# Optimization experiments

Hardware: AMD Instinct MI355X
Metric: run time of the kernel (lower is better)

The kernel has to match this reference:

```python
import jax, jax.numpy as jnp
import numpy as np

T = 16          # timesteps
BATCH = 8       # video clips -> leading dim of x is BATCH*T = 128
C_IN = 768      # fixed by nn.Conv2d(768, redu_dim, 1)
D = 256         # redu_dim
K = 64          # num_centers
H = W = 28
EPS = 1e-12     # torch F.normalize eps


def _conv(x, w, padding):
    # x: [N,C,H,W], w: [O,I,kh,kw]
    return jax.lax.conv_general_dilated(
        x, w, window_strides=(1, 1), padding=padding,
        dimension_numbers=('NCHW', 'OIHW', 'NCHW'))


def setup_inputs() -> dict:
    key = jax.random.key(0)
    ks = jax.random.split(key, 9)
    x = jax.random.normal(ks[0], (BATCH * T, C_IN, H, W), dtype=jnp.float32)
    redu_w = jax.random.normal(ks[1], (D, C_IN, 1, 1), jnp.float32) * 0.02
    redu_b = jnp.zeros((D,), jnp.float32)
    share_w = jax.random.normal(ks[2], (K, D, 1, 1), jnp.float32) * 0.05
    share_b = jnp.zeros((K,), jnp.float32)
    U_z = jax.random.normal(ks[3], (K, K, 3, 3), jnp.float32) * 0.04
    U_r = jax.random.normal(ks[4], (K, K, 3, 3), jnp.float32) * 0.04
    U_h = jax.random.normal(ks[5], (K, K, 3, 3), jnp.float32) * 0.04
    centers = jax.random.normal(ks[6], (K, D), jnp.float32) * 0.06
    return {"x": x, "redu_w": redu_w, "redu_b": redu_b,
            "share_w": share_w, "share_b": share_b,
            "U_z": U_z, "U_r": U_r, "U_h": U_h,
            "centers": centers, "timesteps": T}


def reference(x, redu_w, redu_b, share_w, share_b, U_z, U_r, U_h, centers, timesteps):
    t = timesteps
    bt, _, h, w = x.shape
    b = bt // t
    k = share_w.shape[0]
    d = redu_w.shape[0]

    # channel reduction (1x1 conv)
    xr = _conv(x, redu_w, 'VALID') + redu_b[None, :, None, None]        # [bt,d,h,w]
    # shared assignment logits (1x1 conv)
    wxb = _conv(xr, share_w, 'VALID') + share_b[None, :, None, None]     # [bt,k,h,w]
    wxb = wxb.reshape(b, t, k, h, w).transpose(1, 0, 2, 3, 4)            # [t,b,k,h,w]

    # sequential ConvGRU over timesteps
    h0 = jnp.zeros((b, k, h, w), x.dtype)
    def step(h_tm1, w_t):
        z = jax.nn.sigmoid(w_t + _conv(h_tm1, U_z, 'SAME'))
        r = jax.nn.sigmoid(w_t + _conv(h_tm1, U_r, 'SAME'))
        hh = jnp.tanh(w_t + _conv(r * h_tm1, U_h, 'SAME'))
        h_new = (1.0 - z) * hh + z * h_tm1
        return h_new, h_new
    _, hs = jax.lax.scan(step, h0, wxb)                                  # [t,b,k,h,w]

    assign = hs.transpose(1, 0, 2, 3, 4).reshape(b * t, k, h * w)        # [bt,k,hw]
    # softmax over centers per spatial location
    assign = jax.nn.softmax(assign, axis=1)

    # VLAD aggregation
    a_sum = assign.sum(axis=-1, keepdims=True)                           # [bt,k,1]
    a = a_sum * centers[None]                                            # [bt,k,d]
    xf = xr.reshape(b * t, d, h * w)                                     # [bt,d,hw]
    vlad = jnp.einsum('bkp,bdp->bkd', assign, xf) - a                    # [bt,k,d]

    vlad = vlad.reshape(b, t, k, d).sum(axis=1)                          # [b,k,d]
    # intra-norm over feature dim, then global L2 norm
    vlad = vlad / jnp.maximum(jnp.linalg.norm(vlad, axis=2, keepdims=True), EPS)
    vlad = vlad.reshape(b, k * d)
    vlad = vlad / jnp.maximum(jnp.linalg.norm(vlad, axis=1, keepdims=True), EPS)
    return vlad
```

## Files before the change

### kernel.cpp

```cpp
#include <hip/hip_runtime.h>
#include <hip/hip_bf16.h>

#define T_ 16
#define B_ 8
#define CIN 768
#define D_ 256
#define K_ 64
#define HW 784
#define W_ 28

typedef short short8 __attribute__((ext_vector_type(8)));
typedef short short4v __attribute__((ext_vector_type(4)));
typedef float floatx4 __attribute__((ext_vector_type(4)));
typedef unsigned short ushort_t;

__device__ __forceinline__ unsigned short f2bf(float x) {
    union { float f; unsigned u; } v; v.f = x;
    unsigned u = v.u;
    unsigned r = (u + 0x7fffu + ((u >> 16) & 1u)) >> 16;
    return (unsigned short)r;
}
__device__ __forceinline__ float bf2f(unsigned short h) {
    union { unsigned u; float f; } v; v.u = ((unsigned)h) << 16; return v.f;
}

__device__ __forceinline__ float block_reduce_sum_256(float v) {
    for (int off = 32; off > 0; off >>= 1) v += __shfl_down(v, off, 64);
    __shared__ float red[4];
    __shared__ float tot;
    int lane = threadIdx.x & 63, wid = threadIdx.x >> 6;
    if (lane == 0) red[wid] = v;
    __syncthreads();
    if (threadIdx.x == 0) tot = red[0] + red[1] + red[2] + red[3];
    __syncthreads();
    return tot;
}

__global__ __launch_bounds__(256) void cvt_weights(
    const float* __restrict__ rw, const float* __restrict__ sw,
    const float* __restrict__ Uz, const float* __restrict__ Ur,
    const float* __restrict__ Uh,
    ushort_t* __restrict__ whi, ushort_t* __restrict__ wlo,
    ushort_t* __restrict__ shi, ushort_t* __restrict__ slo,
    ushort_t* __restrict__ azh, ushort_t* __restrict__ azl,
    ushort_t* __restrict__ ahh, ushort_t* __restrict__ ahl)
{
    int i = blockIdx.x * 256 + threadIdx.x;
    const int nR = D_ * CIN;
    const int nS = K_ * D_;
    const int nZR = 128 * 576;
    const int nH = 64 * 576;
    if (i < nR) {
        float x = rw[i];
        unsigned short h = f2bf(x);
        whi[i] = h; wlo[i] = f2bf(x - bf2f(h));
    } else if (i < nR + nS) {
        int j = i - nR;
        float x = sw[j];
        unsigned short h = f2bf(x);
        shi[j] = h; slo[j] = f2bf(x - bf2f(h));
    } else if (i < nR + nS + nZR) {
        int j = i - nR - nS;
        int row = j / 576, kk = j - row * 576;
        int tap = kk >> 6, c = kk & 63;
        const float* U = (row < 64) ? Uz : Ur;
        float x = U[(((size_t)(row & 63)) * 64 + c) * 9 + tap];
        unsigned short h = f2bf(x);
        azh[j] = h; azl[j] = f2bf(x - bf2f(h));
    } else if (i < nR + nS + nZR + nH) {
        int j = i - nR - nS - nZR;
        int row = j / 576, kk = j - row * 576;
        int tap = kk >> 6, c = kk & 63;
        float x = Uh[(((size_t)row) * 64 + c) * 9 + tap];
        unsigned short h = f2bf(x);
        ahh[j] = h; ahl[j] = f2bf(x - bf2f(h));
    }
}

template<int BM, int KD>
__global__ __launch_bounds__(256, 2) void mfma_conv1x1(
    const float* __restrict__ X, const ushort_t* __restrict__ Whi,
    const ushort_t* __restrict__ Wlo, const float* __restrict__ bias,
    float* __restrict__ Out)
{
    const int nt = blockIdx.x, bt = blockIdx.z;
    const int p0 = nt * 112;
    const int tid = threadIdx.x, lane = tid & 63, wv = tid >> 6;
    const float* Xb = X + (size_t)bt * KD * HW;
    float* Ob = Out + (size_t)bt * BM * HW;

    __shared__ ushort_t lB[2][112 * 40];

    constexpr int NI = (BM == 256) ? 7 : 2;
    constexpr int NKS = KD / 32;
    floatx4 acc[4][NI];
#pragma unroll
    for (int a = 0; a < 4; ++a)
#pragma unroll
        for (int b = 0; b < NI; ++b) acc[a][b] = (floatx4){0.f, 0.f, 0.f, 0.f};

    const int koff = (lane >> 4) * 8;
    const int li = lane & 15;
    const int mbase = (BM == 256) ? wv * 64 : 0;

    const int u0j = tid / 112, u0p = tid - u0j * 112;
    const bool u1v = tid < 192;
    const int u1j = (tid + 256) / 112, u1p = (tid + 256) - u1j * 112;

    float b0[16], b1[16];
    short8 ahi[4], alo[4];

    auto loadB = [&](int k0, float* bb) {
        const float* xp0 = Xb + (size_t)(k0 + u0j * 8) * HW + p0 + u0p;
#pragma unroll
        for (int c = 0; c < 8; ++c) bb[c] = xp0[c * HW];
        if (u1v) {
            const float* xp1 = Xb + (size_t)(k0 + u1j * 8) * HW + p0 + u1p;
#pragma unroll
            for (int c = 0; c < 8; ++c) bb[8 + c] = xp1[c * HW];
        }
    };
    auto writeB = [&](const float* bb) {
        short8 vh, vl;
#pragma unroll
        for (int c = 0; c < 8; ++c) {
            unsigned short h = f2bf(bb[c]);
            vh[c] = (short)h; vl[c] = (short)f2bf(bb[c] - bf2f(h));
        }
        *(short8*)&lB[0][u0p * 40 + u0j * 8] = vh;
        *(short8*)&lB[1][u0p * 40 + u0j * 8] = vl;
        if (u1v) {
#pragma unroll
            for (int c = 0; c < 8; ++c) {
                unsigned short h = f2bf(bb[8 + c]);
                vh[c] = (short)h; vl[c] = (short)f2bf(bb[8 + c] - bf2f(h));
            }
            *(short8*)&lB[0][u1p * 40 + u1j * 8] = vh;
            *(short8*)&lB[1][u1p * 40 + u1j * 8] = vl;
        }
    };
    auto loadA = [&](int k0) {
#pragma unroll
        for (int mi = 0; mi < 4; ++mi) {
            int m = mbase + mi * 16 + li;
            ahi[mi] = *(const short8*)(Whi + (size_t)m * KD + k0 + koff);
            alo[mi] = *(const short8*)(Wlo + (size_t)m * KD + k0 + koff);
        }
    };
    auto domfma = [&]() {
        if constexpr (BM == 256) {
#pragma unroll
            for (int ni = 0; ni < 7; ++ni) {
                int n = ni * 16 + li;
                short8 bhi = *(const short8*)&lB[0][n * 40 + koff];
                short8 blo = *(const short8*)&lB[1][n * 40 + koff];
#pragma unroll
                for (int mi = 0; mi < 4; ++mi) {
                    acc[mi][ni] = __builtin_amdgcn_mfma_f32_16x16x32_bf16(ahi[mi], bhi, acc[mi][ni], 0, 0, 0);
                    acc[mi][ni] = __builtin_amdgcn_mfma_f32_16x16x32_bf16(ahi[mi], blo, acc[mi][ni], 0, 0, 0);
                    acc[mi][ni] = __builtin_amdgcn_mfma_f32_16x16x32_bf16(alo[mi], bhi, acc[mi][ni], 0, 0, 0);
                }
            }
        } else {
#pragma unroll
            for (int nj = 0; nj < 2; ++nj) {
                int ni = wv * 2 + nj;
                if (ni >= 7) break;
                int n = ni * 16 + li;
                short8 bhi = *(const short8*)&lB[0][n * 40 + koff];
                short8 blo = *(const short8*)&lB[1][n * 40 + koff];
#pragma unroll
                for (int mi = 0; mi < 4; ++mi) {
                    acc[mi][nj] = __builtin_amdgcn_mfma_f32_16x16x32_bf16(ahi[mi], bhi, acc[mi][nj], 0, 0, 0);
                    acc[mi][nj] = __builtin_amdgcn_mfma_f32_16x16x32_bf16(ahi[mi], blo, acc[mi][nj], 0, 0, 0);
                    acc[mi][nj] = __builtin_amdgcn_mfma_f32_16x16x32_bf16(alo[mi], bhi, acc[mi][nj], 0, 0, 0);
                }
            }
        }
    };

    loadB(0, b0);
    for (int ks = 0; ks < NKS; ks += 2) {
        loadA(ks * 32);
        writeB(b0);
        __syncthreads();
        if (ks + 1 < NKS) loadB((ks + 1) * 32, b1);
        domfma();
        __syncthreads();
        loadA((ks + 1) * 32);
        writeB(b1);
        __syncthreads();
        if (ks + 2 < NKS) loadB((ks + 2) * 32, b0);
        domfma();
        __syncthreads();
    }

    if constexpr (BM == 256) {
#pragma unroll
        for (int mi = 0; mi < 4; ++mi) {
            int m0g = wv * 64 + mi * 16 + ((lane >> 4) << 2);
#pragma unroll
            for (int ni = 0; ni < 7; ++ni) {
                int p = p0 + ni * 16 + li;
#pragma unroll
                for (int r = 0; r < 4; ++r)
                    Ob[(size_t)(m0g + r) * HW + p] = acc[mi][ni][r] + bias[m0g + r];
            }
        }
    } else {
#pragma unroll
        for (int nj = 0; nj < 2; ++nj) {
            int ni = wv * 2 + nj;
            if (ni >= 7) break;
            int p = p0 + ni * 16 + li;
#pragma unroll
            for (int mi = 0; mi < 4; ++mi) {
                int m0g = mi * 16 + ((lane >> 4) << 2);
#pragma unroll
                for (int r = 0; r < 4; ++r)
                    Ob[(size_t)(m0g + r) * HW + p] = acc[mi][nj][r] + bias[m0g + r];
            }
        }
    }
}

__global__ __launch_bounds__(512, 2) void gru_step(
    const ushort_t* __restrict__ hRhi, const ushort_t* __restrict__ hRlo,
    ushort_t* __restrict__ hWhi, ushort_t* __restrict__ hWlo,
    const ushort_t* __restrict__ azh, const ushort_t* __restrict__ azl,
    const ushort_t* __restrict__ ahh, const ushort_t* __restrict__ ahl,
    const float* __restrict__ wxb, float* __restrict__ hs_t, int t)
{
    const int y0 = blockIdx.x, b = blockIdx.y;
    const int tid = threadIdx.x, lane = tid & 63, wv = tid >> 6;
    const int li = lane & 15, koff8 = (lane >> 4) * 8, kq = (lane >> 4) * 4;

    __shared__ ushort_t Hhi[5 * 30 * 72], Hlo[5 * 30 * 72];
    __shared__ ushort_t Rhi[3 * 30 * 72], Rlo[3 * 30 * 72];
    __shared__ float zs[28 * 68];

    {
        const ushort_t* gh = hRhi + (size_t)b * HW * 64;
        const ushort_t* gl = hRlo + (size_t)b * HW * 64;
        for (int e = tid; e < 1200; e += 512) {
            int r = e / 240, rem = e - r * 240;
            int lx = rem >> 3, j = rem & 7;
            int gy = y0 - 2 + r, gx = lx - 1;
            short8 vh = {0,0,0,0,0,0,0,0}, vl = {0,0,0,0,0,0,0,0};
            if (gy >= 0 && gy < 28 && gx >= 0 && gx < 28) {
                size_t go = ((size_t)(gy * 28 + gx)) * 64 + j * 8;
                vh = *(const short8*)(gh + go);
                vl = *(const short8*)(gl + go);
            }
            int lo = (r * 30 + lx) * 72 + j * 8;
            *(short8*)&Hhi[lo] = vh;
            *(short8*)&Hlo[lo] = vl;
        }
        short8 z8 = {0,0,0,0,0,0,0,0};
        for (int e = tid; e < 1620; e += 512) {
            if (e < 810) *(short8*)&Rhi[e * 8] = z8;
            else         *(short8*)&Rlo[(e - 810) * 8] = z8;
        }
    }
    __syncthreads();

    const float* wx = wxb + ((size_t)(b * T_ + t) * K_) * HW;
    const int c0 = li;
    const int c1 = (li < 12) ? 16 + li : 0;

    if (wv < 4) {
        const int kb = wv * 16;
        const ushort_t* Ah = azh + (size_t)(kb + li) * 576;
        const ushort_t* Al = azl + (size_t)(kb + li) * 576;
        floatx4 az[2];
        az[0] = (floatx4){0.f,0.f,0.f,0.f}; az[1] = (floatx4){0.f,0.f,0.f,0.f};
#pragma unroll
        for (int tap = 0; tap < 9; ++tap) {
            const int dy = tap / 3, dx = tap - dy * 3;
#pragma unroll
            for (int ch = 0; ch < 2; ++ch) {
                short8 whi_ = *(const short8*)(Ah + tap * 64 + ch * 32 + koff8);
                short8 wlo_ = *(const short8*)(Al + tap * 64 + ch * 32 + koff8);
                int cb = ch * 32 + koff8;
                int o0 = ((dy + 1) * 30 + c0 + dx) * 72 + cb;
                int o1 = ((dy + 1) * 30 + c1 + dx) * 72 + cb;
                short8 bh0 = *(const short8*)&Hhi[o0];
                short8 bl0 = *(const short8*)&Hlo[o0];
                short8 bh1 = *(const short8*)&Hhi[o1];
                short8 bl1 = *(const short8*)&Hlo[o1];
                az[0] = __builtin_amdgcn_mfma_f32_16x16x32_bf16(whi_, bh0, az[0], 0, 0, 0);
                az[0] = __builtin_amdgcn_mfma_f32_16x16x32_bf16(whi_, bl0, az[0], 0, 0, 0);
                az[0] = __builtin_amdgcn_mfma_f32_16x16x32_bf16(wlo_, bh0, az[0], 0, 0, 0);
                az[1] = __builtin_amdgcn_mfma_f32_16x16x32_bf16(whi_, bh1, az[1], 0, 0, 0);
                az[1] = __builtin_amdgcn_mfma_f32_16x16x32_bf16(whi_, bl1, az[1], 0, 0, 0);
                az[1] = __builtin_amdgcn_mfma_f32_16x16x32_bf16(wlo_, bh1, az[1], 0, 0, 0);
            }
        }
        const int kb4 = kb + kq;
#pragma unroll
        for (int cf = 0; cf < 2; ++cf) {
            int c = cf * 16 + li;
            if (c < 28) {
                floatx4 zv;
#pragma unroll
                for (int r = 0; r < 4; ++r)
                    zv[r] = 1.f / (1.f + __expf(-(wx[(size_t)(kb4 + r) * HW + y0 * 28 + c] + az[cf][r])));
                *(floatx4*)&zs[c * 68 + kb4] = zv;
            }
        }
    } else {
        const int kb = (wv - 4) * 16;
        const ushort_t* Ah = azh + (size_t)(64 + kb + li) * 576;
        const ushort_t* Al = azl + (size_t)(64 + kb + li) * 576;
        floatx4 ar[3][2];
#pragma unroll
        for (int i = 0; i < 3; ++i) {
            ar[i][0] = (floatx4){0.f,0.f,0.f,0.f};
            ar[i][1] = (floatx4){0.f,0.f,0.f,0.f};
        }
#pragma unroll
        for (int tap = 0; tap < 9; ++tap) {
            const int dy = tap / 3, dx = tap - dy * 3;
#pragma unroll
            for (int ch = 0; ch < 2; ++ch) {
                short8 whi_ = *(const short8*)(Ah + tap * 64 + ch * 32 + koff8);
                short8 wlo_ = *(const short8*)(Al + tap * 64 + ch * 32 + koff8);
                int cb = ch * 32 + koff8;
#pragma unroll
                for (int rr = 0; rr < 3; ++rr) {
                    int o0 = ((rr + dy) * 30 + c0 + dx) * 72 + cb;
                    int o1 = ((rr + dy) * 30 + c1 + dx) * 72 + cb;
                    short8 bh0 = *(const short8*)&Hhi[o0];
                    short8 bl0 = *(const short8*)&Hlo[o0];
                    short8 bh1 = *(const short8*)&Hhi[o1];
                    short8 bl1 = *(const short8*)&Hlo[o1];
                    ar[rr][0] = __builtin_amdgcn_mfma_f32_16x16x32_bf16(whi_, bh0, ar[rr][0], 0, 0, 0);
                    ar[rr][0] = __builtin_amdgcn_mfma_f32_16x16x32_bf16(whi_, bl0, ar[rr][0], 0, 0, 0);
                    ar[rr][0] = __builtin_amdgcn_mfma_f32_16x16x32_bf16(wlo_, bh0, ar[rr][0], 0, 0, 0);
                    ar[rr][1] = __builtin_amdgcn_mfma_f32_16x16x32_bf16(whi_, bh1, ar[rr][1], 0, 0, 0);
                    ar[rr][1] = __builtin_amdgcn_mfma_f32_16x16x32_bf16(whi_, bl1, ar[rr][1], 0, 0, 0);
                    ar[rr][1] = __builtin_amdgcn_mfma_f32_16x16x32_bf16(wlo_, bh1, ar[rr][1], 0, 0, 0);
                }
            }
        }
        const int kb4 = kb + kq;
#pragma unroll
        for (int rr = 0; rr < 3; ++rr) {
            int gy = y0 - 1 + rr;
            if (gy < 0 || gy >= 28) continue;
#pragma unroll
            for (int cf = 0; cf < 2; ++cf) {
                int c = cf * 16 + li;
                if (c >= 28) continue;
                short4v ph = *(const short4v*)&Hhi[((rr + 1) * 30 + c + 1) * 72 + kb4];
                short4v pl = *(const short4v*)&Hlo[((rr + 1) * 30 + c + 1) * 72 + kb4];
                short4v vh, vl;
#pragma unroll
                for (int r = 0; r < 4; ++r) {
                    float rv = 1.f / (1.f + __expf(-(wx[(size_t)(kb4 + r) * HW + gy * 28 + c] + ar[rr][cf][r])));
                    float hv = bf2f((unsigned short)ph[r]) + bf2f((unsigned short)pl[r]);
                    float rh = rv * hv;
                    unsigned short h = f2bf(rh);
                    vh[r] = (short)h; vl[r] = (short)f2bf(rh - bf2f(h));
                }
                *(short4v*)&Rhi[(rr * 30 + c + 1) * 72 + kb4] = vh;
                *(short4v*)&Rlo[(rr * 30 + c + 1) * 72 + kb4] = vl;
            }
        }
    }
    __syncthreads();

    if (wv < 4) {
        const int kb = wv * 16;
        const ushort_t* Ah = ahh + (size_t)(kb + li) * 576;
        const ushort_t* Al = ahl + (size_t)(kb + li) * 576;
        floatx4 ac[2];
        ac[0] = (floatx4){0.f,0.f,0.f,0.f}; ac[1] = (floatx4){0.f,0.f,0.f,0.f};
#pragma unroll
        for (int tap = 0; tap < 9; ++tap) {
            const int dy = tap / 3, dx = tap - dy * 3;
#pragma unroll
            for (int ch = 0; ch < 2; ++ch) {
                short8 whi_ = *(const short8*)(Ah + tap * 64 + ch * 32 + koff8);
                short8 wlo_ = *(const short8*)(Al + tap * 64 + ch * 32 + koff8);
                int cb = ch * 32 + koff8;
                int o0 = (dy * 30 + c0 + dx) * 72 + cb;
                int o1 = (dy * 30 + c1 + dx) * 72 + cb;
                short8 bh0 = *(const short8*)&Rhi[o0];
                short8 bl0 = *(const short8*)&Rlo[o0];
                short8 bh1 = *(const short8*)&Rhi[o1];
                short8 bl1 = *(const short8*)&Rlo[o1];
                ac[0] = __builtin_amdgcn_mfma_f32_16x16x32_bf16(whi_, bh0, ac[0], 0, 0, 0);
                ac[0] = __builtin_amdgcn_mfma_f32_16x16x32_bf16(whi_, bl0, ac[0], 0, 0, 0);
                ac[0] = __builtin_amdgcn_mfma_f32_16x16x32_bf16(wlo_, bh0, ac[0], 0, 0, 0);
                ac[1] = __builtin_amdgcn_mfma_f32_16x16x32_bf16(whi_, bh1, ac[1], 0, 0, 0);
                ac[1] = __builtin_amdgcn_mfma_f32_16x16x32_bf16(whi_, bl1, ac[1], 0, 0, 0);
                ac[1] = __builtin_amdgcn_mfma_f32_16x16x32_bf16(wlo_, bh1, ac[1], 0, 0, 0);
            }
        }
        const int kb4 = kb + kq;
        float* hsb = hs_t + (size_t)b * K_ * HW;
#pragma unroll
        for (int cf = 0; cf < 2; ++cf) {
            int c = cf * 16 + li;
            if (c >= 28) continue;
            int p = y0 * 28 + c;
            floatx4 zv = *(const floatx4*)&zs[c * 68 + kb4];
            short4v ph = *(const short4v*)&Hhi[(2 * 30 + c + 1) * 72 + kb4];
            short4v pl = *(const short4v*)&Hlo[(2 * 30 + c + 1) * 72 + kb4];
            short4v vh, vl;
#pragma unroll
            for (int r = 0; r < 4; ++r) {
                int k = kb4 + r;
                float xv = wx[(size_t)k * HW + p] + ac[cf][r];
                float e2 = __expf(2.f * xv);
                float th = 1.f - 2.f / (e2 + 1.f);
                float hp = bf2f((unsigned short)ph[r]) + bf2f((unsigned short)pl[r]);
                float hn = (1.f - zv[r]) * th + zv[r] * hp;
                hsb[(size_t)k * HW + p] = hn;
                unsigned short h = f2bf(hn);
                vh[r] = (short)h; vl[r] = (short)f2bf(hn - bf2f(h));
            }
            size_t o = ((size_t)(b * HW) + p) * 64 + kb4;
            *(short4v*)(hWhi + o) = vh;
            *(short4v*)(hWlo + o) = vl;
        }
    }
}

__global__ __launch_bounds__(256) void softmax_k(float* __restrict__ hs)
{
    int q = blockIdx.x;
    int py = blockIdx.y;
    float* base = hs + (size_t)q * K_ * HW;
    for (int p = py * 392 + threadIdx.x; p < (py + 1) * 392 && p < HW; p += 256) {
        float v[64];
        float m = -1e30f;
#pragma unroll
        for (int k = 0; k < 64; ++k) {
            v[k] = base[(size_t)k * HW + p];
            m = fmaxf(m, v[k]);
        }
        float s = 0.f;
#pragma unroll
        for (int k = 0; k < 64; ++k) {
            v[k] = __expf(v[k] - m);
            s += v[k];
        }
        float inv = 1.f / s;
#pragma unroll
        for (int k = 0; k < 64; ++k)
            base[(size_t)k * HW + p] = v[k] * inv;
    }
}

__global__ __launch_bounds__(256) void asum_k(const float* __restrict__ hs,
                                              float* __restrict__ asum)
{
    int bid = blockIdx.x; int b = bid >> 6, k = bid & 63;
    float s = 0.f;
    for (int t = 0; t < T_; ++t) {
        const float* row = hs + (((size_t)t * B_ + b) * K_ + k) * HW;
        for (int p = threadIdx.x; p < HW; p += 256) s += row[p];
    }
    float tot = block_reduce_sum_256(s);
    if (threadIdx.x == 0) asum[bid] = tot;
}

__global__ __launch_bounds__(256) void vlad_k(const float* __restrict__ assign,
    const float* __restrict__ xr, float* __restrict__ vladt)
{
    int dt = blockIdx.x, t = blockIdx.y, b = blockIdx.z;
    int q = t * B_ + b, bt = b * T_ + t, d0 = dt * 64;
    const float* ab = assign + (size_t)q * K_ * HW;
    const float* xb = xr + (size_t)bt * D_ * HW;
    __shared__ float As[16][68];
    __shared__ float Xs[16][68];
    int tx = threadIdx.x & 15, ty = threadIdx.x >> 4;
    float acc[4][4] = {{0.f}};

    for (int p0 = 0; p0 < HW; p0 += 16) {
#pragma unroll
        for (int it = 0; it < 4; ++it) {
            int e = threadIdx.x + it * 256;
            int row = e >> 4, pp = e & 15;
            As[pp][row] = ab[(size_t)row * HW + p0 + pp];
            Xs[pp][row] = xb[(size_t)(d0 + row) * HW + p0 + pp];
        }
        __syncthreads();
#pragma unroll
        for (int pp = 0; pp < 16; ++pp) {
            float4 a = *(const float4*)&As[pp][ty * 4];
            float4 xv = *(const float4*)&Xs[pp][tx * 4];
            float av[4] = {a.x, a.y, a.z, a.w};
            float xvv[4] = {xv.x, xv.y, xv.z, xv.w};
#pragma unroll
            for (int r = 0; r < 4; ++r)
#pragma unroll
                for (int s = 0; s < 4; ++s)
                    acc[r][s] = fmaf(av[r], xvv[s], acc[r][s]);
        }
        __syncthreads();
    }
#pragma unroll
    for (int r = 0; r < 4; ++r) {
        int k = ty * 4 + r;
        float4 o = {acc[r][0], acc[r][1], acc[r][2], acc[r][3]};
        *(float4*)&vladt[((size_t)bt * K_ + k) * D_ + d0 + tx * 4] = o;
    }
}

__global__ __launch_bounds__(256) void norm1_k(const float* __restrict__ vladt,
    const float* __restrict__ asum, const float* __restrict__ centers,
    float* __restrict__ out)
{
    int bid = blockIdx.x; int b = bid >> 6, k = bid & 63; int d = threadIdx.x;
    float acc = 0.f;
#pragma unroll
    for (int t = 0; t < T_; ++t)
        acc += vladt[(((size_t)b * T_ + t) * K_ + k) * D_ + d];
    acc -= asum[bid] * centers[(size_t)k * D_ + d];
    float ss = block_reduce_sum_256(acc * acc);
    float n = fmaxf(sqrtf(ss), 1e-12f);
    out[((size_t)b * K_ + k) * D_ + d] = acc / n;
}

__global__ __launch_bounds__(256) void norm2_k(float* __restrict__ out)
{
    int b = blockIdx.x;
    float* v = out + (size_t)b * (K_ * D_);
    float s = 0.f;
    for (int i = threadIdx.x; i < K_ * D_; i += 256) {
        float x = v[i];
        s = fmaf(x, x, s);
    }
    float tot = block_reduce_sum_256(s);
    float n = fmaxf(sqrtf(tot), 1e-12f);
    for (int i = threadIdx.x; i < K_ * D_; i += 256) v[i] = v[i] / n;
}

extern "C" void kernel_launch(void* const* d_in, const int* in_sizes, int n_in,
                              void* d_out, int out_size, void* d_ws, size_t ws_size,
                              hipStream_t stream)
{
    const float* x       = (const float*)d_in[0];
    const float* redu_w  = (const float*)d_in[1];
    const float* redu_b  = (const float*)d_in[2];
    const float* share_w = (const float*)d_in[3];
    const float* share_b = (const float*)d_in[4];
    const float* Uz      = (const float*)d_in[5];
    const float* Ur      = (const float*)d_in[6];
    const float* Uh      = (const float*)d_in[7];
    const float* centers = (const float*)d_in[8];

    float* ws = (float*)d_ws;
    const size_t SZ_XR   = (size_t)128 * D_ * HW;
    const size_t SZ_WXB  = (size_t)128 * K_ * HW;
    const size_t SZ_HS   = (size_t)T_ * B_ * K_ * HW;
    const size_t SZ_PLANE= (size_t)B_ * K_ * HW;

    float* xr    = ws;
    float* wxb   = xr + SZ_XR;
    float* hs    = wxb + SZ_WXB;
    float* asumb = hs + SZ_HS;
    float* wsplit= asumb + 512;
    float* area  = wsplit + 323584;

    ushort_t* whi = (ushort_t*)wsplit;
    ushort_t* wlo = whi + 196608;
    ushort_t* shi = wlo + 196608;
    ushort_t* slo = shi + 16384;
    ushort_t* azh = slo + 16384;
    ushort_t* azl = azh + 73728;
    ushort_t* ahh = azl + 73728;
    ushort_t* ahl = ahh + 36864;

    float* vladt = area;
    ushort_t* st = (ushort_t*)area;
    ushort_t* h0hi = st;
    ushort_t* h0lo = st + SZ_PLANE;
    ushort_t* h1hi = st + 2 * SZ_PLANE;
    ushort_t* h1lo = st + 3 * SZ_PLANE;

    hipMemsetAsync(h0hi, 0, 2 * SZ_PLANE * sizeof(ushort_t), stream);

    cvt_weights<<<dim3((D_ * CIN + K_ * D_ + 128 * 576 + 64 * 576 + 255) / 256),
                  256, 0, stream>>>(redu_w, share_w, Uz, Ur, Uh,
                                    whi, wlo, shi, slo, azh, azl, ahh, ahl);

    mfma_conv1x1<256, CIN><<<dim3(7, 1, 128), 256, 0, stream>>>(x, whi, wlo, redu_b, xr);
    mfma_conv1x1<64, D_><<<dim3(7, 1, 128), 256, 0, stream>>>(xr, shi, slo, share_b, wxb);

    for (int t = 0; t < T_; ++t) {
        const ushort_t* rh_ = (t & 1) ? h1hi : h0hi;
        const ushort_t* rl_ = (t & 1) ? h1lo : h0lo;
        ushort_t* wh_ = (t & 1) ? h0hi : h1hi;
        ushort_t* wl_ = (t & 1) ? h0lo : h1lo;
        gru_step<<<dim3(28, 8), 512, 0, stream>>>(rh_, rl_, wh_, wl_,
                                                  azh, azl, ahh, ahl,
                                                  wxb, hs + (size_t)t * SZ_PLANE, t);
    }

    softmax_k<<<dim3(128, 2), 256, 0, stream>>>(hs);
    asum_k<<<512, 256, 0, stream>>>(hs, asumb);

    vlad_k<<<dim3(4, 16, 8), 256, 0, stream>>>(hs, xr, vladt);
    norm1_k<<<512, 256, 0, stream>>>(vladt, asumb, centers, (float*)d_out);
    norm2_k<<<8, 256, 0, stream>>>((float*)d_out);
}
```

Baseline: 674.2 us.

## Double-buffer LDS in 1x1 conv GEMM, retile warps, fuse assignment sums into VLAD

The 1x1 conv GEMM now uses a double-buffered shared tile, so the next K-slice is written while MFMAs run on the current one, which halves the barriers per step. The first conv runs 512 threads with each wave owning 32 output rows across all 7 column tiles, and the second conv now gives each wave 16 rows across all columns instead of splitting columns. The separate asum kernel is removed: per-(bt,k) assignment sums are accumulated inside vlad_k when dt==0 and reduced over time in norm1_k. The changes cost more shared memory and register pressure, and the higher occupancy target in launch bounds may cause spills.

```diff
diff --git a/kernel.cpp b/kernel.cpp
--- a/kernel.cpp
+++ b/kernel.cpp
@@ -77,8 +77,8 @@
     }
 }
 
-template<int BM, int KD>
-__global__ __launch_bounds__(256, 2) void mfma_conv1x1(
+template<int BM, int THR, int KD>
+__global__ __launch_bounds__(THR, 4) void mfma_conv1x1(
     const float* __restrict__ X, const ushort_t* __restrict__ Whi,
     const ushort_t* __restrict__ Wlo, const float* __restrict__ bias,
     float* __restrict__ Out)
@@ -86,140 +86,106 @@
     const int nt = blockIdx.x, bt = blockIdx.z;
     const int p0 = nt * 112;
     const int tid = threadIdx.x, lane = tid & 63, wv = tid >> 6;
+    const int li = lane & 15, koff = (lane >> 4) * 8;
+    constexpr int NWAVE = THR / 64;
+    constexpr int MI = BM / (NWAVE * 16);
+    constexpr int NKS = KD / 32;
+    constexpr int UPT = (THR == 512) ? 1 : 2;
     const float* Xb = X + (size_t)bt * KD * HW;
     float* Ob = Out + (size_t)bt * BM * HW;
 
-    __shared__ ushort_t lB[2][112 * 40];
-
-    constexpr int NI = (BM == 256) ? 7 : 2;
-    constexpr int NKS = KD / 32;
-    floatx4 acc[4][NI];
-#pragma unroll
-    for (int a = 0; a < 4; ++a)
-#pragma unroll
-        for (int b = 0; b < NI; ++b) acc[a][b] = (floatx4){0.f, 0.f, 0.f, 0.f};
-
-    const int koff = (lane >> 4) * 8;
-    const int li = lane & 15;
-    const int mbase = (BM == 256) ? wv * 64 : 0;
-
-    const int u0j = tid / 112, u0p = tid - u0j * 112;
-    const bool u1v = tid < 192;
-    const int u1j = (tid + 256) / 112, u1p = (tid + 256) - u1j * 112;
-
-    float b0[16], b1[16];
-    short8 ahi[4], alo[4];
+    __shared__ ushort_t lB[2][2][112 * 40];
+
+    floatx4 acc[MI][7];
+#pragma unroll
+    for (int a = 0; a < MI; ++a)
+#pragma unroll
+        for (int b = 0; b < 7; ++b) acc[a][b] = (floatx4){0.f, 0.f, 0.f, 0.f};
+
+    float bA[8 * UPT], bB[8 * UPT];
+    short8 ahi[MI], alo[MI];
 
     auto loadB = [&](int k0, float* bb) {
-        const float* xp0 = Xb + (size_t)(k0 + u0j * 8) * HW + p0 + u0p;
-#pragma unroll
-        for (int c = 0; c < 8; ++c) bb[c] = xp0[c * HW];
-        if (u1v) {
-            const float* xp1 = Xb + (size_t)(k0 + u1j * 8) * HW + p0 + u1p;
-#pragma unroll
-            for (int c = 0; c < 8; ++c) bb[8 + c] = xp1[c * HW];
+#pragma unroll
+        for (int u = 0; u < UPT; ++u) {
+            int uu = tid + u * THR;
+            if (uu < 448) {
+                int j = uu / 112, pp = uu - j * 112;
+                const float* xp = Xb + (size_t)(k0 + j * 8) * HW + p0 + pp;
+#pragma unroll
+                for (int c = 0; c < 8; ++c) bb[u * 8 + c] = xp[(size_t)c * HW];
+            }
         }
     };
-    auto writeB = [&](const float* bb) {
-        short8 vh, vl;
-#pragma unroll
-        for (int c = 0; c < 8; ++c) {
-            unsigned short h = f2bf(bb[c]);
-            vh[c] = (short)h; vl[c] = (short)f2bf(bb[c] - bf2f(h));
-        }
-        *(short8*)&lB[0][u0p * 40 + u0j * 8] = vh;
-        *(short8*)&lB[1][u0p * 40 + u0j * 8] = vl;
-        if (u1v) {
-#pragma unroll
-            for (int c = 0; c < 8; ++c) {
-                unsigned short h = f2bf(bb[8 + c]);
-                vh[c] = (short)h; vl[c] = (short)f2bf(bb[8 + c] - bf2f(h));
-            }
-            *(short8*)&lB[0][u1p * 40 + u1j * 8] = vh;
-            *(short8*)&lB[1][u1p * 40 + u1j * 8] = vl;
+    auto writeB = [&](const float* bb, int wb) {
+#pragma unroll
+        for (int u = 0; u < UPT; ++u) {
+            int uu = tid + u * THR;
+            if (uu < 448) {
+                int j = uu / 112, pp = uu - j * 112;
+                short8 vh, vl;
+#pragma unroll
+                for (int c = 0; c < 8; ++c) {
+                    unsigned short h = f2bf(bb[u * 8 + c]);
+                    vh[c] = (short)h; vl[c] = (short)f2bf(bb[u * 8 + c] - bf2f(h));
+                }
+                *(short8*)&lB[wb][0][pp * 40 + j * 8] = vh;
+                *(short8*)&lB[wb][1][pp * 40 + j * 8] = vl;
+            }
         }
     };
     auto loadA = [&](int k0) {
 #pragma unroll
-        for (int mi = 0; mi < 4; ++mi) {
-            int m = mbase + mi * 16 + li;
+        for (int mi = 0; mi < MI; ++mi) {
+            int m = wv * (MI * 16) + mi * 16 + li;
             ahi[mi] = *(const short8*)(Whi + (size_t)m * KD + k0 + koff);
             alo[mi] = *(const short8*)(Wlo + (size_t)m * KD + k0 + koff);
         }
     };
-    auto domfma = [&]() {
-        if constexpr (BM == 256) {
-#pragma unroll
-            for (int ni = 0; ni < 7; ++ni) {
-                int n = ni * 16 + li;
-                short8 bhi = *(const short8*)&lB[0][n * 40 + koff];
-                short8 blo = *(const short8*)&lB[1][n * 40 + koff];
-#pragma unroll
-                for (int mi = 0; mi < 4; ++mi) {
-                    acc[mi][ni] = __builtin_amdgcn_mfma_f32_16x16x32_bf16(ahi[mi], bhi, acc[mi][ni], 0, 0, 0);
-                    acc[mi][ni] = __builtin_amdgcn_mfma_f32_16x16x32_bf16(ahi[mi], blo, acc[mi][ni], 0, 0, 0);
-                    acc[mi][ni] = __builtin_amdgcn_mfma_f32_16x16x32_bf16(alo[mi], bhi, acc[mi][ni], 0, 0, 0);
-                }
-            }
-        } else {
-#pragma unroll
-            for (int nj = 0; nj < 2; ++nj) {
-                int ni = wv * 2 + nj;
-                if (ni >= 7) break;
-                int n = ni * 16 + li;
-                short8 bhi = *(const short8*)&lB[0][n * 40 + koff];
-                short8 blo = *(const short8*)&lB[1][n * 40 + koff];
-#pragma unroll
-                for (int mi = 0; mi < 4; ++mi) {
-                    acc[mi][nj] = __builtin_amdgcn_mfma_f32_16x16x32_bf16(ahi[mi], bhi, acc[mi][nj], 0, 0, 0);
-                    acc[mi][nj] = __builtin_amdgcn_mfma_f32_16x16x32_bf16(ahi[mi], blo, acc[mi][nj], 0, 0, 0);
-                    acc[mi][nj] = __builtin_amdgcn_mfma_f32_16x16x32_bf16(alo[mi], bhi, acc[mi][nj], 0, 0, 0);
-                }
+    auto domfma = [&](int rb) {
+        const ushort_t* bh = &lB[rb][0][0];
+        const ushort_t* bl = &lB[rb][1][0];
+#pragma unroll
+        for (int ni = 0; ni < 7; ++ni) {
+            int n = ni * 16 + li;
+            short8 bhi = *(const short8*)&bh[n * 40 + koff];
+            short8 blo = *(const short8*)&bl[n * 40 + koff];
+#pragma unroll
+            for (int mi = 0; mi < MI; ++mi) {
+                acc[mi][ni] = __builtin_amdgcn_mfma_f32_16x16x32_bf16(ahi[mi], bhi, acc[mi][ni], 0, 0, 0);
+                acc[mi][ni] = __builtin_amdgcn_mfma_f32_16x16x32_bf16(ahi[mi], blo, acc[mi][ni], 0, 0, 0);
+                acc[mi][ni] = __builtin_amdgcn_mfma_f32_16x16x32_bf16(alo[mi], bhi, acc[mi][ni], 0, 0, 0);
             }
         }
     };
 
-    loadB(0, b0);
+    loadB(0, bA);
+    writeB(bA, 0);
+    loadB(32, bB);
+    __syncthreads();
+
     for (int ks = 0; ks < NKS; ks += 2) {
         loadA(ks * 32);
-        writeB(b0);
-        __syncthreads();
-        if (ks + 1 < NKS) loadB((ks + 1) * 32, b1);
-        domfma();
+        if (ks + 1 < NKS) writeB(bB, 1);
+        if (ks + 2 < NKS) loadB((ks + 2) * 32, bA);
+        domfma(0);
         __syncthreads();
         loadA((ks + 1) * 32);
-        writeB(b1);
+        if (ks + 2 < NKS) writeB(bA, 0);
+        if (ks + 3 < NKS) loadB((ks + 3) * 32, bB);
+        domfma(1);
         __syncthreads();
-        if (ks + 2 < NKS) loadB((ks + 2) * 32, b0);
-        domfma();
-        __syncthreads();
-    }
-
-    if constexpr (BM == 256) {
-#pragma unroll
-        for (int mi = 0; mi < 4; ++mi) {
-            int m0g = wv * 64 + mi * 16 + ((lane >> 4) << 2);
-#pragma unroll
-            for (int ni = 0; ni < 7; ++ni) {
-                int p = p0 + ni * 16 + li;
-#pragma unroll
-                for (int r = 0; r < 4; ++r)
-                    Ob[(size_t)(m0g + r) * HW + p] = acc[mi][ni][r] + bias[m0g + r];
-            }
-        }
-    } else {
-#pragma unroll
-        for (int nj = 0; nj < 2; ++nj) {
-            int ni = wv * 2 + nj;
-            if (ni >= 7) break;
+    }
+
+#pragma unroll
+    for (int mi = 0; mi < MI; ++mi) {
+        int m0g = wv * (MI * 16) + mi * 16 + ((lane >> 4) << 2);
+#pragma unroll
+        for (int ni = 0; ni < 7; ++ni) {
             int p = p0 + ni * 16 + li;
 #pragma unroll
-            for (int mi = 0; mi < 4; ++mi) {
-                int m0g = mi * 16 + ((lane >> 4) << 2);
-#pragma unroll
-                for (int r = 0; r < 4; ++r)
-                    Ob[(size_t)(m0g + r) * HW + p] = acc[mi][nj][r] + bias[m0g + r];
-            }
+            for (int r = 0; r < 4; ++r)
+                Ob[(size_t)(m0g + r) * HW + p] = acc[mi][ni][r] + bias[m0g + r];
         }
     }
 }
@@ -454,21 +420,9 @@
     }
 }
 
-__global__ __launch_bounds__(256) void asum_k(const float* __restrict__ hs,
-                                              float* __restrict__ asum)
-{
-    int bid = blockIdx.x; int b = bid >> 6, k = bid & 63;
-    float s = 0.f;
-    for (int t = 0; t < T_; ++t) {
-        const float* row = hs + (((size_t)t * B_ + b) * K_ + k) * HW;
-        for (int p = threadIdx.x; p < HW; p += 256) s += row[p];
-    }
-    float tot = block_reduce_sum_256(s);
-    if (threadIdx.x == 0) asum[bid] = tot;
-}
-
 __global__ __launch_bounds__(256) void vlad_k(const float* __restrict__ assign,
-    const float* __restrict__ xr, float* __restrict__ vladt)
+    const float* __restrict__ xr, float* __restrict__ vladt,
+    float* __restrict__ asum_bt)
 {
     int dt = blockIdx.x, t = blockIdx.y, b = blockIdx.z;
     int q = t * B_ + b, bt = b * T_ + t, d0 = dt * 64;
@@ -478,13 +432,16 @@
     __shared__ float Xs[16][68];
     int tx = threadIdx.x & 15, ty = threadIdx.x >> 4;
     float acc[4][4] = {{0.f}};
+    float pacc[4] = {0.f, 0.f, 0.f, 0.f};
 
     for (int p0 = 0; p0 < HW; p0 += 16) {
 #pragma unroll
         for (int it = 0; it < 4; ++it) {
             int e = threadIdx.x + it * 256;
             int row = e >> 4, pp = e & 15;
-            As[pp][row] = ab[(size_t)row * HW + p0 + pp];
+            float av_ = ab[(size_t)row * HW + p0 + pp];
+            As[pp][row] = av_;
+            if (dt == 0) pacc[it] += av_;
             Xs[pp][row] = xb[(size_t)(d0 + row) * HW + p0 + pp];
         }
         __syncthreads();
@@ -508,10 +465,19 @@
         float4 o = {acc[r][0], acc[r][1], acc[r][2], acc[r][3]};
         *(float4*)&vladt[((size_t)bt * K_ + k) * D_ + d0 + tx * 4] = o;
     }
+    if (dt == 0) {
+#pragma unroll
+        for (int it = 0; it < 4; ++it) {
+            float s = pacc[it];
+#pragma unroll
+            for (int off = 1; off < 16; off <<= 1) s += __shfl_xor(s, off, 16);
+            if (tx == 0) asum_bt[(size_t)bt * 64 + ty + it * 16] = s;
+        }
+    }
 }
 
 __global__ __launch_bounds__(256) void norm1_k(const float* __restrict__ vladt,
-    const float* __restrict__ asum, const float* __restrict__ centers,
+    const float* __restrict__ asum_bt, const float* __restrict__ centers,
     float* __restrict__ out)
 {
     int bid = blockIdx.x; int b = bid >> 6, k = bid & 63; int d = threadIdx.x;
@@ -519,7 +485,11 @@
 #pragma unroll
     for (int t = 0; t < T_; ++t)
         acc += vladt[(((size_t)b * T_ + t) * K_ + k) * D_ + d];
-    acc -= asum[bid] * centers[(size_t)k * D_ + d];
+    float asum = 0.f;
+#pragma unroll
+    for (int t = 0; t < T_; ++t)
+        asum += asum_bt[(size_t)(b * T_ + t) * 64 + k];
+    acc -= asum * centers[(size_t)k * D_ + d];
     float ss = block_reduce_sum_256(acc * acc);
     float n = fmaxf(sqrtf(ss), 1e-12f);
     out[((size_t)b * K_ + k) * D_ + d] = acc / n;
@@ -559,12 +529,12 @@
     const size_t SZ_HS   = (size_t)T_ * B_ * K_ * HW;
     const size_t SZ_PLANE= (size_t)B_ * K_ * HW;
 
-    float* xr    = ws;
-    float* wxb   = xr + SZ_XR;
-    float* hs    = wxb + SZ_WXB;
-    float* asumb = hs + SZ_HS;
-    float* wsplit= asumb + 512;
-    float* area  = wsplit + 323584;
+    float* xr     = ws;
+    float* wxb    = xr + SZ_XR;
+    float* hs     = wxb + SZ_WXB;
+    float* asum_bt= hs + SZ_HS;
+    float* wsplit = asum_bt + 8192;
+    float* area   = wsplit + 323584;
 
     ushort_t* whi = (ushort_t*)wsplit;
     ushort_t* wlo = whi + 196608;
@@ -588,8 +558,8 @@
                   256, 0, stream>>>(redu_w, share_w, Uz, Ur, Uh,
                                     whi, wlo, shi, slo, azh, azl, ahh, ahl);
 
-    mfma_conv1x1<256, CIN><<<dim3(7, 1, 128), 256, 0, stream>>>(x, whi, wlo, redu_b, xr);
-    mfma_conv1x1<64, D_><<<dim3(7, 1, 128), 256, 0, stream>>>(xr, shi, slo, share_b, wxb);
+    mfma_conv1x1<256, 512, CIN><<<dim3(7, 1, 128), 512, 0, stream>>>(x, whi, wlo, redu_b, xr);
+    mfma_conv1x1<64, 256, D_><<<dim3(7, 1, 128), 256, 0, stream>>>(xr, shi, slo, share_b, wxb);
 
     for (int t = 0; t < T_; ++t) {
         const ushort_t* rh_ = (t & 1) ? h1hi : h0hi;
@@ -602,9 +572,8 @@
     }
 
     softmax_k<<<dim3(128, 2), 256, 0, stream>>>(hs);
-    asum_k<<<512, 256, 0, stream>>>(hs, asumb);
-
-    vlad_k<<<dim3(4, 16, 8), 256, 0, stream>>>(hs, xr, vladt);
-    norm1_k<<<512, 256, 0, stream>>>(vladt, asumb, centers, (float*)d_out);
+
+    vlad_k<<<dim3(4, 16, 8), 256, 0, stream>>>(hs, xr, vladt, asum_bt);
+    norm1_k<<<512, 256, 0, stream>>>(vladt, asum_bt, centers, (float*)d_out);
     norm2_k<<<8, 256, 0, stream>>>((float*)d_out);
 }
```

After: 684.3 us. About the same (+1.5%).
